# Kernel optimization log

Measured on AMD Instinct MI355X. Metric: run time of the kernel, lower is better.

## Reference

```python
import jax, jax.numpy as jnp
import numpy as np

NC = 100000   # n cells
NG = 8000     # n genes
D = 128       # h_dim
E_CG, E_GC, E_CC, E_GG = 1500000, 1500000, 1000000, 200000
SLOPE = 0.05  # LeakyReLU negative slope
LN_EPS = 1e-5


def setup_inputs() -> dict:
    key = jax.random.key(0)
    ks = jax.random.split(key, 16)
    f32 = jnp.float32
    inp = {
        "h_cell": jax.random.normal(ks[0], (NC, D), f32),
        "h_gene": jax.random.normal(ks[1], (NG, D), f32),
        "src_cg": jax.random.randint(ks[2], (E_CG,), 0, NC),
        "dst_cg": jax.random.randint(ks[3], (E_CG,), 0, NG),
        "src_gc": jax.random.randint(ks[4], (E_GC,), 0, NG),
        "dst_gc": jax.random.randint(ks[5], (E_GC,), 0, NC),
        "src_cc": jax.random.randint(ks[6], (E_CC,), 0, NC),
        "dst_cc": jax.random.randint(ks[7], (E_CC,), 0, NC),
        "src_gg": jax.random.randint(ks[8], (E_GG,), 0, NG),
        "dst_gg": jax.random.randint(ks[9], (E_GG,), 0, NG),
        "W_cg": jax.random.normal(ks[10], (D, D), f32) * (1.0 / np.sqrt(D)),
        "W_gc": jax.random.normal(ks[11], (D, D), f32) * (1.0 / np.sqrt(D)),
        "W_cc": jax.random.normal(ks[12], (D, D), f32) * (1.0 / np.sqrt(D)),
        "W_gg": jax.random.normal(ks[13], (D, D), f32) * (1.0 / np.sqrt(D)),
        "b_cell": jnp.zeros((D,), f32),
        "b_gene": jnp.zeros((D,), f32),
        "ln_s_cell": jnp.ones((D,), f32),
        "ln_b_cell": jnp.zeros((D,), f32),
        "ln_s_gene": jnp.ones((D,), f32),
        "ln_b_gene": jnp.zeros((D,), f32),
    }
    return inp


def _rel_conv(h_src, W, src, dst, n_dst):
    # per-relation GraphConv, norm='right': transform, gather, scatter-sum, / in-degree
    m = (h_src @ W)[src]                                   # [E, D]
    agg = jax.ops.segment_sum(m, dst, num_segments=n_dst)  # [n_dst, D]
    deg = jax.ops.segment_sum(jnp.ones(dst.shape, m.dtype), dst, num_segments=n_dst)
    return agg / jnp.clip(deg, 1.0)[:, None]


def _layernorm(x, s, b):
    mu = jnp.mean(x, axis=-1, keepdims=True)
    var = jnp.var(x, axis=-1, keepdims=True)
    return (x - mu) * jax.lax.rsqrt(var + LN_EPS) * s + b


def _leaky(x):
    return jnp.where(x >= 0, x, SLOPE * x)


def _shared_layer(hc, hg, idx, p):
    # aggregate='sum' over relations targeting each dst ntype, then bias, act, LN
    oc = (_rel_conv(hg, p["W_gc"], idx["src_gc"], idx["dst_gc"], NC)
          + _rel_conv(hc, p["W_cc"], idx["src_cc"], idx["dst_cc"], NC)
          + p["b_cell"])
    og = (_rel_conv(hc, p["W_cg"], idx["src_cg"], idx["dst_cg"], NG)
          + _rel_conv(hg, p["W_gg"], idx["src_gg"], idx["dst_gg"], NG)
          + p["b_gene"])
    oc = _layernorm(_leaky(oc), p["ln_s_cell"], p["ln_b_cell"])
    og = _layernorm(_leaky(og), p["ln_s_gene"], p["ln_b_gene"])
    return oc, og


def reference(h_cell, h_gene, src_cg, dst_cg, src_gc, dst_gc, src_cc, dst_cc,
              src_gg, dst_gg, W_cg, W_gc, W_cc, W_gg, b_cell, b_gene,
              ln_s_cell, ln_b_cell, ln_s_gene, ln_b_gene):
    idx = dict(src_cg=src_cg, dst_cg=dst_cg, src_gc=src_gc, dst_gc=dst_gc,
               src_cc=src_cc, dst_cc=dst_cc, src_gg=src_gg, dst_gg=dst_gg)
    p = dict(W_cg=W_cg, W_gc=W_gc, W_cc=W_cc, W_gg=W_gg,
             b_cell=b_cell, b_gene=b_gene,
             ln_s_cell=ln_s_cell, ln_b_cell=ln_b_cell,
             ln_s_gene=ln_s_gene, ln_b_gene=ln_b_gene)
    hc, hg = h_cell, h_gene
    for _ in range(2):  # num_hidden_layers=2, SAME shared layer both times
        hc, hg = _shared_layer(hc, hg, idx, p)
    # pack the heterogeneous output dict as one array: [NC+NG, D]
    return jnp.concatenate([hc, hg], axis=0)
```

## Files before the change

### kernel.cpp

```cpp
#include <hip/hip_runtime.h>
#include <hip/hip_bf16.h>

#define NCELL 100000
#define NGENE 8000
#define DIM   128
#define NE_CG 1500000
#define NE_GC 1500000
#define NE_CC 1000000
#define NE_GG 200000
#define SLOPE 0.05f
#define LN_EPS 1e-5f

typedef __attribute__((ext_vector_type(8))) short bf16x8;
typedef __attribute__((ext_vector_type(4))) float f32x4;

__device__ __forceinline__ float bflo(unsigned v) { return __uint_as_float(v << 16); }
__device__ __forceinline__ float bfhi(unsigned v) { return __uint_as_float(v & 0xffff0000u); }
__device__ __forceinline__ unsigned short f2bf(float x) {
    union { float f; unsigned u; } a; a.f = x;
    unsigned r = a.u + 0x7fffu + ((a.u >> 16) & 1u);
    return (unsigned short)(r >> 16);
}
__device__ __forceinline__ unsigned pack2(float x, float y) {
    return (unsigned)f2bf(x) | ((unsigned)f2bf(y) << 16);
}

__global__ __launch_bounds__(256)
void conv2_k(const float* __restrict__ inc, unsigned short* __restrict__ outc,
             const float* __restrict__ ing, unsigned short* __restrict__ outg,
             int cellBlocks, int n2c, int n2g) {
    const float* in; unsigned short* out; int i, n2;
    if ((int)blockIdx.x < cellBlocks) {
        in = inc; out = outc; n2 = n2c; i = blockIdx.x * 256 + threadIdx.x;
    } else {
        in = ing; out = outg; n2 = n2g; i = (blockIdx.x - cellBlocks) * 256 + threadIdx.x;
    }
    if (i < n2) {
        float2 v = ((const float2*)in)[i];
        ((unsigned*)out)[i] = pack2(v.x, v.y);
    }
}

__global__ void pack2_w_k(const float* __restrict__ WAc, const float* __restrict__ WBc,
                          unsigned short* __restrict__ Wpc,
                          const float* __restrict__ WAg, const float* __restrict__ WBg,
                          unsigned short* __restrict__ Wpg) {
    int bb = blockIdx.x;
    const float *WA, *WB; unsigned short* Wp;
    if (bb < 64) { WA = WAc; WB = WBc; Wp = Wpc; }
    else { bb -= 64; WA = WAg; WB = WBg; Wp = Wpg; }
    int lane = threadIdx.x;
    int t = bb >> 3, c = bb & 7;
    int n = t * 16 + (lane & 15);
    int k0 = c * 32 + (lane >> 4) * 8;
    #pragma unroll
    for (int j = 0; j < 8; ++j) {
        int k = k0 + j;
        float x = (k < 128) ? WA[k * 128 + n] : WB[(k - 128) * 128 + n];
        Wp[((size_t)(bb * 64 + lane)) * 8 + j] = f2bf(x);
    }
}

struct RelP {
    const int* src; const int* dst; int n; int shift;
    int nbins; int N; int cap;
    int* deg; int* offg; int* bkt;
    int* bcur; unsigned* stg;
    int cblk0;
    int sblk0;
};

__global__ __launch_bounds__(256)
void bin_fill4_k(RelP r0, RelP r1, RelP r2, RelP r3) {
    int b = blockIdx.x;
    RelP R = (b >= r3.cblk0) ? r3 : (b >= r2.cblk0) ? r2 : (b >= r1.cblk0) ? r1 : r0;
    int lb = b - R.cblk0;
    __shared__ int cnt[512];
    __shared__ int basem[512];
    int tid = threadIdx.x;
    cnt[tid] = 0; cnt[tid + 256] = 0;
    __syncthreads();
    int base = lb * 4096;
    int bins[16]; int ranks[16]; unsigned pk[16];
    #pragma unroll
    for (int it = 0; it < 16; ++it) {
        int i = base + it * 256 + tid;
        bins[it] = -1;
        if (i < R.n) {
            int d = R.dst[i];
            int bn = d >> R.shift;
            int dl = d & ((1 << R.shift) - 1);
            bins[it] = bn;
            pk[it] = (unsigned)R.src[i] | ((unsigned)dl << 20);
            ranks[it] = atomicAdd(&cnt[bn], 1);
        }
    }
    __syncthreads();
    if (cnt[tid])       basem[tid]       = atomicAdd(&R.bcur[tid],       cnt[tid]);
    if (cnt[tid + 256]) basem[tid + 256] = atomicAdd(&R.bcur[tid + 256], cnt[tid + 256]);
    __syncthreads();
    #pragma unroll
    for (int it = 0; it < 16; ++it)
        if (bins[it] >= 0) {
            int r = basem[bins[it]] + ranks[it];
            if (r >= R.cap) r = R.cap - 1;
            R.stg[(size_t)bins[it] * R.cap + r] = pk[it];
        }
}

__global__ __launch_bounds__(256)
void bin_csr4_k(RelP r0, RelP r1, RelP r2, RelP r3) {
    int b = blockIdx.x;
    RelP R = (b >= r3.sblk0) ? r3 : (b >= r2.sblk0) ? r2 : (b >= r1.sblk0) ? r1 : r0;
    int lb = b - R.sblk0;
    int tid = threadIdx.x;
    int ebase = lb * R.cap;
    int cnt = R.bcur[lb]; if (cnt > R.cap) cnt = R.cap;
    __shared__ int degm[256];
    __shared__ int sc[256];
    __shared__ int cur[256];
    degm[tid] = 0;
    __syncthreads();
    for (int i = tid; i < cnt; i += 256)
        atomicAdd(&degm[(R.stg[ebase + i] >> 20) & 255], 1);
    __syncthreads();
    int x = degm[tid];
    sc[tid] = x;
    __syncthreads();
    for (int ofs = 1; ofs < 256; ofs <<= 1) {
        int t = (tid >= ofs) ? sc[tid - ofs] : 0;
        __syncthreads();
        sc[tid] += t;
        __syncthreads();
    }
    int excl = sc[tid] - x;
    cur[tid] = excl;
    int node = (lb << R.shift) + tid;
    if (tid < (1 << R.shift) && node < R.N) { R.deg[node] = x; R.offg[node] = ebase + excl; }
    __syncthreads();
    for (int i = tid; i < cnt; i += 256) {
        unsigned p = R.stg[ebase + i];
        int dl = (p >> 20) & 255;
        int r = atomicAdd(&cur[dl], 1);
        R.bkt[ebase + r] = (int)(p & 0xFFFFFu);
    }
}

__global__ __launch_bounds__(256)
void gather2_k(const unsigned short* __restrict__ hc, const unsigned short* __restrict__ hg,
               const int* __restrict__ off_gc, const int* __restrict__ deg_gc, const int* __restrict__ bkt_gc,
               const int* __restrict__ off_cc, const int* __restrict__ deg_cc, const int* __restrict__ bkt_cc,
               const int* __restrict__ off_cg, const int* __restrict__ deg_cg, const int* __restrict__ bkt_cg,
               const int* __restrict__ off_gg, const int* __restrict__ deg_gg, const int* __restrict__ bkt_gg,
               unsigned short* __restrict__ Acat_c, unsigned short* __restrict__ Acat_g,
               int cellBlocks) {
    int wave = threadIdx.x >> 6, lane = threadIdx.x & 63;
    int g = lane >> 4, c = lane & 15;
    const unsigned short *hA, *hB;
    const int *offA, *degA, *bktA, *offB, *degB, *bktB;
    unsigned short* Aout; int node, N;
    if ((int)blockIdx.x < cellBlocks) {
        node = blockIdx.x * 4 + wave; N = NCELL;
        hA = hg; offA = off_gc; degA = deg_gc; bktA = bkt_gc;
        hB = hc; offB = off_cc; degB = deg_cc; bktB = bkt_cc;
        Aout = Acat_c;
    } else {
        node = (blockIdx.x - cellBlocks) * 4 + wave; N = NGENE;
        hA = hc; offA = off_cg; degA = deg_cg; bktA = bkt_cg;
        hB = hg; offB = off_gg; degB = deg_gg; bktB = bkt_gg;
        Aout = Acat_g;
    }
    if (node >= N) return;

    int nA = degA[node], sA = offA[node];
    int nB = degB[node], sB = offB[node];
    float aA[8] = {0.f, 0.f, 0.f, 0.f, 0.f, 0.f, 0.f, 0.f};
    float aB[8] = {0.f, 0.f, 0.f, 0.f, 0.f, 0.f, 0.f, 0.f};
    int mx = (nA > nB) ? nA : nB;

    for (int j0 = 0; j0 < mx; j0 += 32) {
        int l32 = lane & 31;
        int jj = j0 + l32;
        int iv = 0;
        if (lane < 32) { if (jj < nA) iv = bktA[sA + jj]; }
        else           { if (jj < nB) iv = bktB[sB + jj]; }
        int mA = nA - j0;
        int mB = nB - j0;
        #pragma unroll
        for (int t = 0; t < 8; ++t) {
            int j = t * 4 + g;
            int sidxA = __shfl(iv, j);
            int sidxB = __shfl(iv, 32 + j);
            if (j < mA) {
                uint4 v = *(const uint4*)(hA + (size_t)sidxA * DIM + c * 8);
                aA[0] += bflo(v.x); aA[1] += bfhi(v.x);
                aA[2] += bflo(v.y); aA[3] += bfhi(v.y);
                aA[4] += bflo(v.z); aA[5] += bfhi(v.z);
                aA[6] += bflo(v.w); aA[7] += bfhi(v.w);
            }
            if (j < mB) {
                uint4 v = *(const uint4*)(hB + (size_t)sidxB * DIM + c * 8);
                aB[0] += bflo(v.x); aB[1] += bfhi(v.x);
                aB[2] += bflo(v.y); aB[3] += bfhi(v.y);
                aB[4] += bflo(v.z); aB[5] += bfhi(v.z);
                aB[6] += bflo(v.w); aB[7] += bfhi(v.w);
            }
        }
    }

    #pragma unroll
    for (int i = 0; i < 8; ++i) {
        aA[i] += __shfl_xor(aA[i], 16); aA[i] += __shfl_xor(aA[i], 32);
        aB[i] += __shfl_xor(aB[i], 16); aB[i] += __shfl_xor(aB[i], 32);
    }
    float invA = 1.0f / fmaxf((float)nA, 1.0f);
    float invB = 1.0f / fmaxf((float)nB, 1.0f);
    uint4* outrow = (uint4*)(Aout + (size_t)node * 256);
    if (g == 0) {
        outrow[c] = make_uint4(pack2(aA[0] * invA, aA[1] * invA), pack2(aA[2] * invA, aA[3] * invA),
                               pack2(aA[4] * invA, aA[5] * invA), pack2(aA[6] * invA, aA[7] * invA));
    } else if (g == 1) {
        outrow[16 + c] = make_uint4(pack2(aB[0] * invB, aB[1] * invB), pack2(aB[2] * invB, aB[3] * invB),
                                    pack2(aB[4] * invB, aB[5] * invB), pack2(aB[6] * invB, aB[7] * invB));
    }
}

#define GBM 128
__global__ __launch_bounds__(256)
void gemm2_ln_k(const unsigned short* __restrict__ Acat_c, const unsigned short* __restrict__ Acat_g,
                const unsigned short* __restrict__ Wp_c, const unsigned short* __restrict__ Wp_g,
                const float* __restrict__ bias_c, const float* __restrict__ bias_g,
                const float* __restrict__ ls_c, const float* __restrict__ lb_c,
                const float* __restrict__ ls_g, const float* __restrict__ lb_g,
                unsigned short* __restrict__ outh_c, unsigned short* __restrict__ outh_g,
                float* __restrict__ outf_c, float* __restrict__ outf_g,
                int cellBlocks) {
    const unsigned short *A, *Wp; const float *bias, *lns, *lnb;
    unsigned short* outh; float* outf; int M, mb;
    if ((int)blockIdx.x < cellBlocks) {
        A = Acat_c; Wp = Wp_c; bias = bias_c; lns = ls_c; lnb = lb_c;
        outh = outh_c; outf = outf_c; M = NCELL; mb = blockIdx.x;
    } else {
        A = Acat_g; Wp = Wp_g; bias = bias_g; lns = ls_g; lnb = lb_g;
        outh = outh_g; outf = outf_g; M = NGENE; mb = blockIdx.x - cellBlocks;
    }
    __shared__ unsigned short Ws[32768];
    int tid = threadIdx.x;
    {
        const uint4* s = (const uint4*)Wp;
        uint4* d = (uint4*)Ws;
        #pragma unroll
        for (int i = tid; i < 4096; i += 256) d[i] = s[i];
    }
    __syncthreads();

    int wave = tid >> 6, lane = tid & 63;
    int col0 = lane & 15;
    int kq = lane >> 4;
    int m_base = mb * GBM + wave * 32;

    f32x4 acc[2][8];
    #pragma unroll
    for (int mt = 0; mt < 2; ++mt)
        #pragma unroll
        for (int t = 0; t < 8; ++t) acc[mt][t] = (f32x4){0.f, 0.f, 0.f, 0.f};

    const unsigned short* Ar0 = A + (size_t)(m_base + col0) * 256 + kq * 8;
    const unsigned short* Ar1 = Ar0 + 16 * 256;
    #pragma unroll
    for (int cc = 0; cc < 8; ++cc) {
        bf16x8 a0 = *(const bf16x8*)(Ar0 + cc * 32);
        bf16x8 a1 = *(const bf16x8*)(Ar1 + cc * 32);
        #pragma unroll
        for (int t = 0; t < 8; ++t) {
            bf16x8 b = *(const bf16x8*)(Ws + ((t * 8 + cc) * 64 + lane) * 8);
            acc[0][t] = __builtin_amdgcn_mfma_f32_16x16x32_bf16(a0, b, acc[0][t], 0, 0, 0);
            acc[1][t] = __builtin_amdgcn_mfma_f32_16x16x32_bf16(a1, b, acc[1][t], 0, 0, 0);
        }
    }

    float bias_r[8], s_r[8], b_r[8];
    #pragma unroll
    for (int t = 0; t < 8; ++t) {
        int col = t * 16 + col0;
        bias_r[t] = bias[col]; s_r[t] = lns[col]; b_r[t] = lnb[col];
    }
    #pragma unroll
    for (int mt = 0; mt < 2; ++mt) {
        #pragma unroll
        for (int r = 0; r < 4; ++r) {
            int row = m_base + mt * 16 + kq * 4 + r;
            float v[8]; float sum = 0.f, sq = 0.f;
            #pragma unroll
            for (int t = 0; t < 8; ++t) {
                float x = acc[mt][t][r] + bias_r[t];
                x = (x >= 0.f) ? x : SLOPE * x;
                v[t] = x; sum += x; sq += x * x;
            }
            #pragma unroll
            for (int ofs = 1; ofs <= 8; ofs <<= 1) {
                sum += __shfl_xor(sum, ofs);
                sq  += __shfl_xor(sq, ofs);
            }
            float mu = sum * (1.0f / 128.0f);
            float var = sq * (1.0f / 128.0f) - mu * mu;
            float rstd = rsqrtf(var + LN_EPS);
            if (row < M) {
                if (outh) {
                    #pragma unroll
                    for (int t = 0; t < 8; ++t)
                        outh[(size_t)row * 128 + t * 16 + col0] =
                            f2bf((v[t] - mu) * rstd * s_r[t] + b_r[t]);
                } else {
                    #pragma unroll
                    for (int t = 0; t < 8; ++t)
                        outf[(size_t)row * 128 + t * 16 + col0] =
                            (v[t] - mu) * rstd * s_r[t] + b_r[t];
                }
            }
        }
    }
}

extern "C" void kernel_launch(void* const* d_in, const int* in_sizes, int n_in,
                              void* d_out, int out_size, void* d_ws, size_t ws_size,
                              hipStream_t stream) {
    const float* h_cell = (const float*)d_in[0];
    const float* h_gene = (const float*)d_in[1];
    const int* src_cg = (const int*)d_in[2];
    const int* dst_cg = (const int*)d_in[3];
    const int* src_gc = (const int*)d_in[4];
    const int* dst_gc = (const int*)d_in[5];
    const int* src_cc = (const int*)d_in[6];
    const int* dst_cc = (const int*)d_in[7];
    const int* src_gg = (const int*)d_in[8];
    const int* dst_gg = (const int*)d_in[9];
    const float* W_cg = (const float*)d_in[10];
    const float* W_gc = (const float*)d_in[11];
    const float* W_cc = (const float*)d_in[12];
    const float* W_gg = (const float*)d_in[13];
    const float* b_cell = (const float*)d_in[14];
    const float* b_gene = (const float*)d_in[15];
    const float* ln_s_cell = (const float*)d_in[16];
    const float* ln_b_cell = (const float*)d_in[17];
    const float* ln_s_gene = (const float*)d_in[18];
    const float* ln_b_gene = (const float*)d_in[19];
    float* out = (float*)d_out;

    const int MPC = ((NCELL + GBM - 1) / GBM) * GBM;
    const int MPG = ((NGENE + GBM - 1) / GBM) * GBM;
    const int NB_C = (NCELL + 255) / 256;
    const int NB_G = (NGENE + 15) / 16;
    const int CAP_GC = 4352;
    const int CAP_CC = 3072;
    const int CAP_CG = 3584;
    const int CAP_GG = 768;

    char* wsb = (char*)d_ws;
    size_t off = 0;
    auto alloc = [&](size_t bytes) -> char* {
        char* p = wsb + off;
        off = (off + bytes + 255) & ~(size_t)255;
        return p;
    };
    unsigned short* Acat_c = (unsigned short*)alloc((size_t)MPC * 256 * 2);
    unsigned short* Acat_g = (unsigned short*)alloc((size_t)MPG * 256 * 2);
    unsigned short* hcb0 = (unsigned short*)alloc((size_t)NCELL * DIM * 2);
    unsigned short* hgb0 = (unsigned short*)alloc((size_t)NGENE * DIM * 2);
    unsigned short* hcb1 = (unsigned short*)alloc((size_t)NCELL * DIM * 2);
    unsigned short* hgb1 = (unsigned short*)alloc((size_t)NGENE * DIM * 2);
    unsigned short* Wp_cell = (unsigned short*)alloc(65536);
    unsigned short* Wp_gene = (unsigned short*)alloc(65536);
    int ndeg = 2 * NCELL + 2 * NGENE;
    int* degs = (int*)alloc((size_t)ndeg * 4);
    int* deg_gc = degs;
    int* deg_cc = degs + NCELL;
    int* deg_cg = degs + 2 * NCELL;
    int* deg_gg = degs + 2 * NCELL + NGENE;
    int* offs = (int*)alloc((size_t)ndeg * 4);
    int* off_gc = offs;
    int* off_cc = offs + NCELL;
    int* off_cg = offs + 2 * NCELL;
    int* off_gg = offs + 2 * NCELL + NGENE;
    int* bkt_gc = (int*)alloc((size_t)NB_C * CAP_GC * 4);
    int* bkt_cc = (int*)alloc((size_t)NB_C * CAP_CC * 4);
    int* bkt_cg = (int*)alloc((size_t)NB_G * CAP_CG * 4);
    int* bkt_gg = (int*)alloc((size_t)NB_G * CAP_GG * 4);
    unsigned* stg_gc = (unsigned*)alloc((size_t)NB_C * CAP_GC * 4);
    unsigned* stg_cc = (unsigned*)alloc((size_t)NB_C * CAP_CC * 4);
    unsigned* stg_cg = (unsigned*)alloc((size_t)NB_G * CAP_CG * 4);
    unsigned* stg_gg = (unsigned*)alloc((size_t)NB_G * CAP_GG * 4);
    int* binmem = (int*)alloc(4 * 512 * 4);

    const int n2c = NCELL * DIM / 2, n2g = NGENE * DIM / 2;
    const int convCB = (n2c + 255) / 256;
    const int convGB = (n2g + 255) / 256;
    conv2_k<<<convCB + convGB, 256, 0, stream>>>(h_cell, hcb0, h_gene, hgb0, convCB, n2c, n2g);
    pack2_w_k<<<128, 64, 0, stream>>>(W_gc, W_cc, Wp_cell, W_cg, W_gg, Wp_gene);

    hipMemsetAsync(binmem, 0, 4 * 512 * 4, stream);
    const int nbk_gc = (NE_GC + 4095) / 4096;
    const int nbk_cc = (NE_CC + 4095) / 4096;
    const int nbk_cg = (NE_CG + 4095) / 4096;
    const int nbk_gg = (NE_GG + 4095) / 4096;
    auto mkrel = [&](const int* s, const int* d, int n, int shift, int nbins, int N, int cap,
                     int* deg, int* offg, int* bkt, int* bm, unsigned* stg,
                     int cblk0, int sblk0) {
        RelP r;
        r.src = s; r.dst = d; r.n = n; r.shift = shift; r.nbins = nbins; r.N = N; r.cap = cap;
        r.deg = deg; r.offg = offg; r.bkt = bkt;
        r.bcur = bm; r.stg = stg;
        r.cblk0 = cblk0; r.sblk0 = sblk0;
        return r;
    };
    RelP r0 = mkrel(src_gc, dst_gc, NE_GC, 8, NB_C, NCELL, CAP_GC, deg_gc, off_gc, bkt_gc,
                    binmem + 0 * 512, stg_gc, 0, 0);
    RelP r1 = mkrel(src_cc, dst_cc, NE_CC, 8, NB_C, NCELL, CAP_CC, deg_cc, off_cc, bkt_cc,
                    binmem + 1 * 512, stg_cc, nbk_gc, NB_C);
    RelP r2 = mkrel(src_cg, dst_cg, NE_CG, 4, NB_G, NGENE, CAP_CG, deg_cg, off_cg, bkt_cg,
                    binmem + 2 * 512, stg_cg, nbk_gc + nbk_cc, 2 * NB_C);
    RelP r3 = mkrel(src_gg, dst_gg, NE_GG, 4, NB_G, NGENE, CAP_GG, deg_gg, off_gg, bkt_gg,
                    binmem + 3 * 512, stg_gg, nbk_gc + nbk_cc + nbk_cg, 2 * NB_C + NB_G);
    const int cntBlocks = nbk_gc + nbk_cc + nbk_cg + nbk_gg;
    const int csrBlocks = 2 * NB_C + 2 * NB_G;
    bin_fill4_k<<<cntBlocks, 256, 0, stream>>>(r0, r1, r2, r3);
    bin_csr4_k<<<csrBlocks, 256, 0, stream>>>(r0, r1, r2, r3);

    const int gatherCB = NCELL / 4;
    const int gatherGB = (NGENE + 3) / 4;
    const int gemmCB = MPC / GBM;
    const int gemmGB = MPG / GBM;
    const unsigned short* hc = hcb0;
    const unsigned short* hg = hgb0;
    for (int layer = 0; layer < 2; ++layer) {
        int final_ = (layer == 1);
        gather2_k<<<gatherCB + gatherGB, 256, 0, stream>>>(
            hc, hg,
            off_gc, deg_gc, bkt_gc, off_cc, deg_cc, bkt_cc,
            off_cg, deg_cg, bkt_cg, off_gg, deg_gg, bkt_gg,
            Acat_c, Acat_g, gatherCB);
        gemm2_ln_k<<<gemmCB + gemmGB, 256, 0, stream>>>(
            Acat_c, Acat_g, Wp_cell, Wp_gene, b_cell, b_gene,
            ln_s_cell, ln_b_cell, ln_s_gene, ln_b_gene,
            final_ ? nullptr : hcb1, final_ ? nullptr : hgb1,
            final_ ? out : nullptr, final_ ? out + (size_t)NCELL * DIM : nullptr,
            gemmCB);
        hc = hcb1;
        hg = hgb1;
    }
}
```

Before: 577.0 us.

## Switch bf16 storage and MFMA to fp16 with packed fp16 gather accumulation

Replaces bf16 storage of activations and weights with fp16 and uses the f16 MFMA variant. The gather now accumulates neighbor sums in packed half2 registers instead of unpacking each value to fp32, which cuts ALU work per loaded element. Gene blocks are also moved ahead of cell blocks so the high-degree gene nodes start first, reducing tail imbalance. The risk is fp16 range and precision loss when summing many neighbors (gene in-degree is around 190) in half precision.

```diff
diff --git a/kernel.cpp b/kernel.cpp
--- a/kernel.cpp
+++ b/kernel.cpp
@@ -1,5 +1,4 @@
 #include <hip/hip_runtime.h>
-#include <hip/hip_bf16.h>
 
 #define NCELL 100000
 #define NGENE 8000
@@ -11,18 +10,19 @@
 #define SLOPE 0.05f
 #define LN_EPS 1e-5f
 
-typedef __attribute__((ext_vector_type(8))) short bf16x8;
+typedef __attribute__((ext_vector_type(2))) _Float16 f16x2;
+typedef __attribute__((ext_vector_type(8))) _Float16 f16x8;
 typedef __attribute__((ext_vector_type(4))) float f32x4;
 
-__device__ __forceinline__ float bflo(unsigned v) { return __uint_as_float(v << 16); }
-__device__ __forceinline__ float bfhi(unsigned v) { return __uint_as_float(v & 0xffff0000u); }
-__device__ __forceinline__ unsigned short f2bf(float x) {
-    union { float f; unsigned u; } a; a.f = x;
-    unsigned r = a.u + 0x7fffu + ((a.u >> 16) & 1u);
-    return (unsigned short)(r >> 16);
-}
-__device__ __forceinline__ unsigned pack2(float x, float y) {
-    return (unsigned)f2bf(x) | ((unsigned)f2bf(y) << 16);
+__device__ __forceinline__ unsigned short f2h(float x) {
+    return __builtin_bit_cast(unsigned short, (_Float16)x);
+}
+__device__ __forceinline__ unsigned pack2h(float x, float y) {
+    f16x2 h = { (_Float16)x, (_Float16)y };
+    return __builtin_bit_cast(unsigned, h);
+}
+__device__ __forceinline__ f16x2 u2h2(unsigned u) {
+    return __builtin_bit_cast(f16x2, u);
 }
 
 __global__ __launch_bounds__(256)
@@ -37,7 +37,7 @@
     }
     if (i < n2) {
         float2 v = ((const float2*)in)[i];
-        ((unsigned*)out)[i] = pack2(v.x, v.y);
+        ((unsigned*)out)[i] = pack2h(v.x, v.y);
     }
 }
 
@@ -57,7 +57,7 @@
     for (int j = 0; j < 8; ++j) {
         int k = k0 + j;
         float x = (k < 128) ? WA[k * 128 + n] : WB[(k - 128) * 128 + n];
-        Wp[((size_t)(bb * 64 + lane)) * 8 + j] = f2bf(x);
+        Wp[((size_t)(bb * 64 + lane)) * 8 + j] = f2h(x);
     }
 }
 
@@ -153,29 +153,31 @@
                const int* __restrict__ off_cg, const int* __restrict__ deg_cg, const int* __restrict__ bkt_cg,
                const int* __restrict__ off_gg, const int* __restrict__ deg_gg, const int* __restrict__ bkt_gg,
                unsigned short* __restrict__ Acat_c, unsigned short* __restrict__ Acat_g,
-               int cellBlocks) {
+               int geneBlocks) {
     int wave = threadIdx.x >> 6, lane = threadIdx.x & 63;
     int g = lane >> 4, c = lane & 15;
     const unsigned short *hA, *hB;
     const int *offA, *degA, *bktA, *offB, *degB, *bktB;
     unsigned short* Aout; int node, N;
-    if ((int)blockIdx.x < cellBlocks) {
-        node = blockIdx.x * 4 + wave; N = NCELL;
+    if ((int)blockIdx.x < geneBlocks) {
+        node = blockIdx.x * 4 + wave; N = NGENE;
+        hA = hc; offA = off_cg; degA = deg_cg; bktA = bkt_cg;
+        hB = hg; offB = off_gg; degB = deg_gg; bktB = bkt_gg;
+        Aout = Acat_g;
+    } else {
+        node = (blockIdx.x - geneBlocks) * 4 + wave; N = NCELL;
         hA = hg; offA = off_gc; degA = deg_gc; bktA = bkt_gc;
         hB = hc; offB = off_cc; degB = deg_cc; bktB = bkt_cc;
         Aout = Acat_c;
-    } else {
-        node = (blockIdx.x - cellBlocks) * 4 + wave; N = NGENE;
-        hA = hc; offA = off_cg; degA = deg_cg; bktA = bkt_cg;
-        hB = hg; offB = off_gg; degB = deg_gg; bktB = bkt_gg;
-        Aout = Acat_g;
     }
     if (node >= N) return;
 
     int nA = degA[node], sA = offA[node];
     int nB = degB[node], sB = offB[node];
-    float aA[8] = {0.f, 0.f, 0.f, 0.f, 0.f, 0.f, 0.f, 0.f};
-    float aB[8] = {0.f, 0.f, 0.f, 0.f, 0.f, 0.f, 0.f, 0.f};
+
+    f16x2 aA[4], aB[4];
+    #pragma unroll
+    for (int i = 0; i < 4; ++i) { aA[i] = (f16x2)(_Float16)0; aB[i] = (f16x2)(_Float16)0; }
     int mx = (nA > nB) ? nA : nB;
 
     for (int j0 = 0; j0 < mx; j0 += 32) {
@@ -193,35 +195,37 @@
             int sidxB = __shfl(iv, 32 + j);
             if (j < mA) {
                 uint4 v = *(const uint4*)(hA + (size_t)sidxA * DIM + c * 8);
-                aA[0] += bflo(v.x); aA[1] += bfhi(v.x);
-                aA[2] += bflo(v.y); aA[3] += bfhi(v.y);
-                aA[4] += bflo(v.z); aA[5] += bfhi(v.z);
-                aA[6] += bflo(v.w); aA[7] += bfhi(v.w);
+                aA[0] += u2h2(v.x); aA[1] += u2h2(v.y);
+                aA[2] += u2h2(v.z); aA[3] += u2h2(v.w);
             }
             if (j < mB) {
                 uint4 v = *(const uint4*)(hB + (size_t)sidxB * DIM + c * 8);
-                aB[0] += bflo(v.x); aB[1] += bfhi(v.x);
-                aB[2] += bflo(v.y); aB[3] += bfhi(v.y);
-                aB[4] += bflo(v.z); aB[5] += bfhi(v.z);
-                aB[6] += bflo(v.w); aB[7] += bfhi(v.w);
+                aB[0] += u2h2(v.x); aB[1] += u2h2(v.y);
+                aB[2] += u2h2(v.z); aB[3] += u2h2(v.w);
             }
         }
     }
 
+    float fA[8], fB[8];
+    #pragma unroll
+    for (int i = 0; i < 4; ++i) {
+        fA[2 * i]     = (float)aA[i][0]; fA[2 * i + 1] = (float)aA[i][1];
+        fB[2 * i]     = (float)aB[i][0]; fB[2 * i + 1] = (float)aB[i][1];
+    }
     #pragma unroll
     for (int i = 0; i < 8; ++i) {
-        aA[i] += __shfl_xor(aA[i], 16); aA[i] += __shfl_xor(aA[i], 32);
-        aB[i] += __shfl_xor(aB[i], 16); aB[i] += __shfl_xor(aB[i], 32);
+        fA[i] += __shfl_xor(fA[i], 16); fA[i] += __shfl_xor(fA[i], 32);
+        fB[i] += __shfl_xor(fB[i], 16); fB[i] += __shfl_xor(fB[i], 32);
     }
     float invA = 1.0f / fmaxf((float)nA, 1.0f);
     float invB = 1.0f / fmaxf((float)nB, 1.0f);
     uint4* outrow = (uint4*)(Aout + (size_t)node * 256);
     if (g == 0) {
-        outrow[c] = make_uint4(pack2(aA[0] * invA, aA[1] * invA), pack2(aA[2] * invA, aA[3] * invA),
-                               pack2(aA[4] * invA, aA[5] * invA), pack2(aA[6] * invA, aA[7] * invA));
+        outrow[c] = make_uint4(pack2h(fA[0] * invA, fA[1] * invA), pack2h(fA[2] * invA, fA[3] * invA),
+                               pack2h(fA[4] * invA, fA[5] * invA), pack2h(fA[6] * invA, fA[7] * invA));
     } else if (g == 1) {
-        outrow[16 + c] = make_uint4(pack2(aB[0] * invB, aB[1] * invB), pack2(aB[2] * invB, aB[3] * invB),
-                                    pack2(aB[4] * invB, aB[5] * invB), pack2(aB[6] * invB, aB[7] * invB));
+        outrow[16 + c] = make_uint4(pack2h(fB[0] * invB, fB[1] * invB), pack2h(fB[2] * invB, fB[3] * invB),
+                                    pack2h(fB[4] * invB, fB[5] * invB), pack2h(fB[6] * invB, fB[7] * invB));
     }
 }
 
@@ -269,13 +273,13 @@
     const unsigned short* Ar1 = Ar0 + 16 * 256;
     #pragma unroll
     for (int cc = 0; cc < 8; ++cc) {
-        bf16x8 a0 = *(const bf16x8*)(Ar0 + cc * 32);
-        bf16x8 a1 = *(const bf16x8*)(Ar1 + cc * 32);
+        f16x8 a0 = *(const f16x8*)(Ar0 + cc * 32);
+        f16x8 a1 = *(const f16x8*)(Ar1 + cc * 32);
         #pragma unroll
         for (int t = 0; t < 8; ++t) {
-            bf16x8 b = *(const bf16x8*)(Ws + ((t * 8 + cc) * 64 + lane) * 8);
-            acc[0][t] = __builtin_amdgcn_mfma_f32_16x16x32_bf16(a0, b, acc[0][t], 0, 0, 0);
-            acc[1][t] = __builtin_amdgcn_mfma_f32_16x16x32_bf16(a1, b, acc[1][t], 0, 0, 0);
+            f16x8 b = *(const f16x8*)(Ws + ((t * 8 + cc) * 64 + lane) * 8);
+            acc[0][t] = __builtin_amdgcn_mfma_f32_16x16x32_f16(a0, b, acc[0][t], 0, 0, 0);
+            acc[1][t] = __builtin_amdgcn_mfma_f32_16x16x32_f16(a1, b, acc[1][t], 0, 0, 0);
         }
     }
 
@@ -310,7 +314,7 @@
                     #pragma unroll
                     for (int t = 0; t < 8; ++t)
                         outh[(size_t)row * 128 + t * 16 + col0] =
-                            f2bf((v[t] - mu) * rstd * s_r[t] + b_r[t]);
+                            f2h((v[t] - mu) * rstd * s_r[t] + b_r[t]);
                 } else {
                     #pragma unroll
                     for (int t = 0; t < 8; ++t)
@@ -434,11 +438,11 @@
     const unsigned short* hg = hgb0;
     for (int layer = 0; layer < 2; ++layer) {
         int final_ = (layer == 1);
-        gather2_k<<<gatherCB + gatherGB, 256, 0, stream>>>(
+        gather2_k<<<gatherGB + gatherCB, 256, 0, stream>>>(
             hc, hg,
             off_gc, deg_gc, bkt_gc, off_cc, deg_cc, bkt_cc,
             off_cg, deg_cg, bkt_cg, off_gg, deg_gg, bkt_gg,
-            Acat_c, Acat_g, gatherCB);
+            Acat_c, Acat_g, gatherGB);
         gemm2_ln_k<<<gemmCB + gemmGB, 256, 0, stream>>>(
             Acat_c, Acat_g, Wp_cell, Wp_gene, b_cell, b_gene,
             ln_s_cell, ln_b_cell, ln_s_gene, ln_b_gene,
```

Result: faster. 520.5 us (-9.8%).
